# Kernel tuning notes

Hardware: AMD Instinct MI355X
Metric: run time of the kernel (lower is better)

The kernel has to match this reference:

```python
import jax, jax.numpy as jnp
import numpy as np

GROUPS = 32
HEADS = 4
EPS_GN = 1e-5
EPS_DEN = 1e-6


def group_norm(x, gamma, beta):
    b, c, h, w = x.shape
    xg = x.reshape(b, GROUPS, (c // GROUPS) * h * w)
    mu = xg.mean(axis=-1, keepdims=True)
    var = xg.var(axis=-1, keepdims=True)
    xn = ((xg - mu) * jax.lax.rsqrt(var + EPS_GN)).reshape(b, c, h, w)
    return xn * gamma[None, :, None, None] + beta[None, :, None, None]


def setup_inputs() -> dict:
    key = jax.random.key(0)
    ks = jax.random.split(key, 4)
    b, c, h, w = 16, 256, 64, 64
    x = jax.random.normal(ks[0], (b, c, h, w), dtype=jnp.float32)
    gamma = jnp.ones((c,), jnp.float32)
    beta = jnp.zeros((c,), jnp.float32)
    w_qkv = jax.random.normal(ks[1], (3 * c, c), jnp.float32) * (1.0 / np.sqrt(c))
    b_qkv = jnp.zeros((3 * c,), jnp.float32)
    w_out = jax.random.normal(ks[2], (c, c), jnp.float32) * (1.0 / np.sqrt(c))
    b_out = jnp.zeros((c,), jnp.float32)
    return {"x": x, "gamma": gamma, "beta": beta, "w_qkv": w_qkv,
            "b_qkv": b_qkv, "w_out": w_out, "b_out": b_out}


def reference(x, gamma, beta, w_qkv, b_qkv, w_out, b_out):
    b, c, h, w = x.shape
    d = c // HEADS
    n = h * w
    xn = group_norm(x, gamma, beta)
    # 1x1 conv == channel GEMM: [b,3c,h,w]
    qkv = jnp.einsum('bchw,oc->bohw', xn, w_qkv) + b_qkv[None, :, None, None]
    q, k, v = jnp.split(qkv, 3, axis=1)
    # b (heads d) h w -> b heads d n
    q = q.reshape(b, HEADS, d, n)
    k = k.reshape(b, HEADS, d, n)
    v = v.reshape(b, HEADS, d, n)
    q = jax.nn.elu(q) + 1.0
    k = jax.nn.elu(k) + 1.0
    k_sum = k.sum(axis=-1)                                 # [b,H,d]
    kv = jnp.einsum('bhdn,bhen->bhde', k, v)               # [b,H,d,d]
    out = jnp.einsum('bhde,bhdn->bhen', kv, q)             # [b,H,d,n]
    denom = jnp.einsum('bhdn,bhd->bhn', q, k_sum)          # [b,H,n]
    out = out / (denom[:, :, None, :] + EPS_DEN)
    out = out.reshape(b, c, h, w)
    out = jnp.einsum('bchw,oc->bohw', out, w_out) + b_out[None, :, None, None]
    return out + x
```

## Files before the change

### kernel.cpp

```cpp
#include <hip/hip_runtime.h>
#include <stdint.h>

#define BATCH 16
#define CH    256
#define NSP   4096
#define NH    4
#define HD    64

typedef __attribute__((ext_vector_type(8))) short bf16x8;
typedef __attribute__((ext_vector_type(4))) float f32x4;
typedef __attribute__((ext_vector_type(4))) unsigned int u32x4;

__device__ __forceinline__ short f2bf(float f) {
    union { float f; unsigned u; } v; v.f = f;
    unsigned r = (v.u + 0x7fffu + ((v.u >> 16) & 1u)) >> 16;
    return (short)r;
}
__device__ __forceinline__ float bf2f(short s) {
    union { float f; unsigned u; } v; v.u = ((unsigned)(unsigned short)s) << 16;
    return v.f;
}

__global__ __launch_bounds__(256) void k_convert_w(
        const float* __restrict__ wq, const float* __restrict__ wo,
        short* __restrict__ wq_bf, short* __restrict__ wo_bf) {
    int i = blockIdx.x * 256 + threadIdx.x;
    if (i < 768 * 256) wq_bf[i] = f2bf(wq[i]);
    if (i < 256 * 256) wo_bf[i] = f2bf(wo[i]);
}

__global__ __launch_bounds__(256) void k_gn_stats(
        const float* __restrict__ x, float* __restrict__ mu, float* __restrict__ rstd) {
    int bg = blockIdx.x;
    const float4* p = (const float4*)(x + (size_t)bg * 32768);
    float s = 0.f, sq = 0.f;
    for (int i = threadIdx.x; i < 8192; i += 256) {
        float4 v = p[i];
        s  += v.x + v.y + v.z + v.w;
        sq += v.x * v.x + v.y * v.y + v.z * v.z + v.w * v.w;
    }
    for (int off = 32; off; off >>= 1) { s += __shfl_down(s, off); sq += __shfl_down(sq, off); }
    __shared__ float ls[4], lq[4];
    int w = threadIdx.x >> 6;
    if ((threadIdx.x & 63) == 0) { ls[w] = s; lq[w] = sq; }
    __syncthreads();
    if (threadIdx.x == 0) {
        float S = ls[0] + ls[1] + ls[2] + ls[3];
        float Q = lq[0] + lq[1] + lq[2] + lq[3];
        float m = S / 32768.f;
        float var = Q / 32768.f - m * m;
        mu[bg] = m; rstd[bg] = rsqrtf(var + 1e-5f);
    }
}

__global__ __launch_bounds__(256) void k_gn_apply(
        const float* __restrict__ x, const float* __restrict__ gamma,
        const float* __restrict__ beta, const float* __restrict__ mu,
        const float* __restrict__ rstd, short* __restrict__ xn_t) {
    int b = blockIdx.y;
    int n0 = blockIdx.x * 64;
    __shared__ short lds[64 * 264];
    __shared__ float smu[32], srstd[32], sg[256], sb[256];
    int t = threadIdx.x;
    if (t < 32) { smu[t] = mu[b * 32 + t]; srstd[t] = rstd[b * 32 + t]; }
    sg[t] = gamma[t]; sb[t] = beta[t];
    __syncthreads();
    int nl4 = (t & 15) * 4, cq = t >> 4;
    const float* xb = x + (size_t)b * CH * NSP;
    for (int cb = 0; cb < 16; cb++) {
        int c = cb * 16 + cq;
        int g = c >> 3;
        float4 v = *(const float4*)(xb + (size_t)c * NSP + n0 + nl4);
        float sc = srstd[g] * sg[c];
        float sh = sb[c] - smu[g] * sc;
        lds[(nl4 + 0) * 264 + c] = f2bf(v.x * sc + sh);
        lds[(nl4 + 1) * 264 + c] = f2bf(v.y * sc + sh);
        lds[(nl4 + 2) * 264 + c] = f2bf(v.z * sc + sh);
        lds[(nl4 + 3) * 264 + c] = f2bf(v.w * sc + sh);
    }
    __syncthreads();
    short* outb = xn_t + ((size_t)b * NSP + n0) * CH;
    #pragma unroll
    for (int i = 0; i < 8; i++) {
        int ch = t + i * 256;
        int row = ch >> 5, cc = (ch & 31) * 8;
        *(u32x4*)(outb + (size_t)row * CH + cc) = *(const u32x4*)(lds + row * 264 + cc);
    }
}

__global__ __launch_bounds__(256) void k_qkv_gemm(
        const short* __restrict__ wq_bf, const float* __restrict__ b_qkv,
        const short* __restrict__ xn_t, short* __restrict__ q_t,
        float* __restrict__ kvT_g, float* __restrict__ ksum_g) {
    int b = blockIdx.z, mt = blockIdx.y, nt = blockIdx.x;
    bool is_q = (mt < 2);
    int h = mt - 2;
    __shared__ union SM {
        struct { short a[128 * 40]; short bm[128 * 40]; } st;
        short c[128 * 136];
    } sm;
    __shared__ float ksred[64];
    int t = threadIdx.x, lane = t & 63, wv = t >> 6;
    int lr = lane & 15, quad = lane >> 4;
    int wm = (wv & 1) * 64, wn = (wv >> 1) * 64;
    f32x4 acc[4][4] = {};
    const short* Bb = xn_t + ((size_t)b * NSP + (size_t)nt * 128) * 256;
    for (int k0 = 0; k0 < 256; k0 += 32) {
        #pragma unroll
        for (int i = 0; i < 2; i++) {
            int ch = t + i * 256;
            int row = ch >> 2, kc = (ch & 3) * 8;
            int grow = is_q ? (mt * 128 + row)
                            : (row < 64 ? 256 + h * 64 + row : 512 + h * 64 + (row - 64));
            *(u32x4*)(sm.st.a  + row * 40 + kc) = *(const u32x4*)(wq_bf + (size_t)grow * 256 + k0 + kc);
            *(u32x4*)(sm.st.bm + row * 40 + kc) = *(const u32x4*)(Bb + (size_t)row * 256 + k0 + kc);
        }
        __syncthreads();
        bf16x8 afr[4], bfr[4];
        #pragma unroll
        for (int mi = 0; mi < 4; mi++) afr[mi] = *(const bf16x8*)(sm.st.a  + (wm + mi * 16 + lr) * 40 + quad * 8);
        #pragma unroll
        for (int ni = 0; ni < 4; ni++) bfr[ni] = *(const bf16x8*)(sm.st.bm + (wn + ni * 16 + lr) * 40 + quad * 8);
        #pragma unroll
        for (int mi = 0; mi < 4; mi++)
            #pragma unroll
            for (int ni = 0; ni < 4; ni++)
                acc[mi][ni] = __builtin_amdgcn_mfma_f32_16x16x32_bf16(afr[mi], bfr[ni], acc[mi][ni], 0, 0, 0);
        __syncthreads();
    }
    if (t < 64) ksred[t] = 0.f;
    #pragma unroll
    for (int mi = 0; mi < 4; mi++)
      #pragma unroll
      for (int ni = 0; ni < 4; ni++)
        #pragma unroll
        for (int r = 0; r < 4; r++) {
            int ol = wm + mi * 16 + quad * 4 + r;
            int nl = wn + ni * 16 + lr;
            int o = is_q ? (mt * 128 + ol)
                         : (ol < 64 ? 256 + h * 64 + ol : 512 + h * 64 + (ol - 64));
            float v = acc[mi][ni][r] + b_qkv[o];
            if (o < 512) v = v > 0.f ? v + 1.f : __expf(v);
            if (is_q) sm.c[nl * 136 + ol] = f2bf(v);
            else      sm.c[ol * 136 + nl] = f2bf(v);
        }
    __syncthreads();
    if (is_q) {
        short* qb = q_t + (size_t)b * NH * NSP * HD;
        #pragma unroll
        for (int i = 0; i < 8; i++) {
            int ch = t + i * 256;
            int row = ch >> 4, c8 = (ch & 15) * 8;
            int hh = mt * 2 + (c8 >> 6), d0 = c8 & 63;
            int n = nt * 128 + row;
            *(u32x4*)(qb + ((size_t)hh * NSP + n) * HD + d0) = *(const u32x4*)(sm.c + row * 136 + c8);
        }
    } else {
        {
            int kd = t >> 2, nc0 = (t & 3) * 32;
            float s = 0.f;
            #pragma unroll
            for (int j = 0; j < 32; j++) s += bf2f(sm.c[kd * 136 + nc0 + j]);
            atomicAdd(&ksred[kd], s);
        }
        f32x4 acc2[4] = {};
        #pragma unroll
        for (int kk = 0; kk < 128; kk += 32) {
            bf16x8 af = *(const bf16x8*)(sm.c + (64 + wv * 16 + lr) * 136 + kk + quad * 8);
            bf16x8 bf[4];
            #pragma unroll
            for (int ni = 0; ni < 4; ni++)
                bf[ni] = *(const bf16x8*)(sm.c + (ni * 16 + lr) * 136 + kk + quad * 8);
            #pragma unroll
            for (int ni = 0; ni < 4; ni++)
                acc2[ni] = __builtin_amdgcn_mfma_f32_16x16x32_bf16(af, bf[ni], acc2[ni], 0, 0, 0);
        }
        __syncthreads();
        int bh = b * NH + h;
        float* kvg = kvT_g + (size_t)bh * 4096;
        #pragma unroll
        for (int ni = 0; ni < 4; ni++)
            #pragma unroll
            for (int r = 0; r < 4; r++) {
                int e = wv * 16 + quad * 4 + r;
                int d = ni * 16 + lr;
                atomicAdd(&kvg[e * 64 + d], acc2[ni][r]);
            }
        if (t < 64) atomicAdd(&ksum_g[bh * 64 + t], ksred[t]);
    }
}

__global__ __launch_bounds__(256) void k_attn(
        const short* __restrict__ q_t, const float* __restrict__ kvT_g,
        const float* __restrict__ ksum_g, short* __restrict__ attn_t) {
    int nt = blockIdx.x, h = blockIdx.y, b = blockIdx.z;
    int bh = b * 4 + h;
    __shared__ short ql[128 * 72];
    __shared__ short kvl[64 * 72];
    __shared__ float ksl[64];
    __shared__ float dnl[128];
    int t = threadIdx.x, lane = t & 63, wv = t >> 6, lr = lane & 15, quad = lane >> 4;
    const short* qb = q_t + ((size_t)bh * NSP + (size_t)nt * 128) * HD;
    #pragma unroll
    for (int i = 0; i < 4; i++) {
        int ch = t + i * 256;
        int row = ch >> 3, dc = (ch & 7) * 8;
        *(u32x4*)(ql + row * 72 + dc) = *(const u32x4*)(qb + (size_t)row * HD + dc);
    }
    const float* kvg = kvT_g + (size_t)bh * 4096;
    for (int i = t; i < 4096; i += 256)
        kvl[(i >> 6) * 72 + (i & 63)] = f2bf(kvg[i]);
    if (t < 64) ksl[t] = ksum_g[bh * 64 + t];
    __syncthreads();
    if (t < 128) {
        float s = 0.f;
        #pragma unroll
        for (int d = 0; d < 64; d++) s += bf2f(ql[t * 72 + d]) * ksl[d];
        dnl[t] = 1.f / (s + 1e-6f);
    }
    __syncthreads();
    f32x4 acc[2][4] = {};
    int mbase = wv * 32;
    #pragma unroll
    for (int kk = 0; kk < 64; kk += 32) {
        bf16x8 afr[2], bfr[4];
        #pragma unroll
        for (int mi = 0; mi < 2; mi++) afr[mi] = *(const bf16x8*)(ql + (mbase + mi * 16 + lr) * 72 + kk + quad * 8);
        #pragma unroll
        for (int ni = 0; ni < 4; ni++) bfr[ni] = *(const bf16x8*)(kvl + (ni * 16 + lr) * 72 + kk + quad * 8);
        #pragma unroll
        for (int mi = 0; mi < 2; mi++)
            #pragma unroll
            for (int ni = 0; ni < 4; ni++)
                acc[mi][ni] = __builtin_amdgcn_mfma_f32_16x16x32_bf16(afr[mi], bfr[ni], acc[mi][ni], 0, 0, 0);
    }
    short* ob = attn_t + ((size_t)b * NSP + (size_t)nt * 128) * CH + h * 64;
    #pragma unroll
    for (int mi = 0; mi < 2; mi++)
      #pragma unroll
      for (int ni = 0; ni < 4; ni++)
        #pragma unroll
        for (int r = 0; r < 4; r++) {
            int nl = mbase + mi * 16 + quad * 4 + r;
            int e = ni * 16 + lr;
            ob[(size_t)nl * CH + e] = f2bf(acc[mi][ni][r] * dnl[nl]);
        }
}

__global__ __launch_bounds__(256) void k_out_gemm(
        const short* __restrict__ wo_bf, const float* __restrict__ b_out,
        const short* __restrict__ attn_t, const float* __restrict__ x,
        float* __restrict__ out) {
    int b = blockIdx.z, mt = blockIdx.y, nt = blockIdx.x;
    __shared__ short lds_a[128 * 40];
    __shared__ short lds_b[128 * 40];
    int t = threadIdx.x, lane = t & 63, wv = t >> 6, lr = lane & 15, quad = lane >> 4;
    int wm = (wv & 1) * 64, wn = (wv >> 1) * 64;
    f32x4 acc[4][4] = {};
    const short* Ab = wo_bf + (size_t)mt * 128 * 256;
    const short* Bb = attn_t + ((size_t)b * NSP + (size_t)nt * 128) * 256;
    for (int k0 = 0; k0 < 256; k0 += 32) {
        #pragma unroll
        for (int i = 0; i < 2; i++) {
            int ch = t + i * 256;
            int row = ch >> 2, kc = (ch & 3) * 8;
            *(u32x4*)(lds_a + row * 40 + kc) = *(const u32x4*)(Ab + (size_t)row * 256 + k0 + kc);
            *(u32x4*)(lds_b + row * 40 + kc) = *(const u32x4*)(Bb + (size_t)row * 256 + k0 + kc);
        }
        __syncthreads();
        bf16x8 afr[4], bfr[4];
        #pragma unroll
        for (int mi = 0; mi < 4; mi++) afr[mi] = *(const bf16x8*)(lds_a + (wm + mi * 16 + lr) * 40 + quad * 8);
        #pragma unroll
        for (int ni = 0; ni < 4; ni++) bfr[ni] = *(const bf16x8*)(lds_b + (wn + ni * 16 + lr) * 40 + quad * 8);
        #pragma unroll
        for (int mi = 0; mi < 4; mi++)
            #pragma unroll
            for (int ni = 0; ni < 4; ni++)
                acc[mi][ni] = __builtin_amdgcn_mfma_f32_16x16x32_bf16(afr[mi], bfr[ni], acc[mi][ni], 0, 0, 0);
        __syncthreads();
    }
    const float* xb = x + ((size_t)b * CH + (size_t)mt * 128) * NSP + (size_t)nt * 128;
    float* outb = out + ((size_t)b * CH + (size_t)mt * 128) * NSP + (size_t)nt * 128;
    #pragma unroll
    for (int mi = 0; mi < 4; mi++)
      #pragma unroll
      for (int ni = 0; ni < 4; ni++)
        #pragma unroll
        for (int r = 0; r < 4; r++) {
            int ol = wm + mi * 16 + quad * 4 + r;
            int nl = wn + ni * 16 + lr;
            int o = mt * 128 + ol;
            outb[(size_t)ol * NSP + nl] = acc[mi][ni][r] + b_out[o] + xb[(size_t)ol * NSP + nl];
        }
}

extern "C" void kernel_launch(void* const* d_in, const int* in_sizes, int n_in,
                              void* d_out, int out_size, void* d_ws, size_t ws_size,
                              hipStream_t stream) {
    const float* x     = (const float*)d_in[0];
    const float* gamma = (const float*)d_in[1];
    const float* beta  = (const float*)d_in[2];
    const float* w_qkv = (const float*)d_in[3];
    const float* b_qkv = (const float*)d_in[4];
    const float* w_out = (const float*)d_in[5];
    const float* b_out = (const float*)d_in[6];
    float* out = (float*)d_out;

    char* ws = (char*)d_ws;
    size_t off = 0;
    float* mu    = (float*)(ws + off); off += 2048;
    float* rstd  = (float*)(ws + off); off += 2048;
    short* wq_bf = (short*)(ws + off); off += (size_t)768 * 256 * 2;
    short* wo_bf = (short*)(ws + off); off += (size_t)256 * 256 * 2;
    short* xn_t  = (short*)(ws + off);
    short* attn_t = xn_t;
    off += (size_t)BATCH * NSP * CH * 2;
    short* q_t   = (short*)(ws + off); off += (size_t)BATCH * NSP * CH * 2;
    float* kvT_g = (float*)(ws + off); off += (size_t)64 * 4096 * 4;
    float* ksum_g = (float*)(ws + off); off += (size_t)64 * 64 * 4;

    if (ws_size < off) return;

    k_convert_w<<<768, 256, 0, stream>>>(w_qkv, w_out, wq_bf, wo_bf);
    k_gn_stats<<<512, 256, 0, stream>>>(x, mu, rstd);
    k_gn_apply<<<dim3(64, 16), 256, 0, stream>>>(x, gamma, beta, mu, rstd, xn_t);
    hipMemsetAsync(kvT_g, 0, (size_t)(64 * 4096 + 64 * 64) * 4, stream);
    k_qkv_gemm<<<dim3(32, 6, 16), 256, 0, stream>>>(wq_bf, b_qkv, xn_t, q_t, kvT_g, ksum_g);
    k_attn<<<dim3(32, 4, 16), 256, 0, stream>>>(q_t, kvT_g, ksum_g, attn_t);
    k_out_gemm<<<dim3(32, 2, 16), 256, 0, stream>>>(wo_bf, b_out, attn_t, x, out);
}
```

Before: 311.1 us.

## Fuse GroupNorm into QKV GEMM and attention into output GEMM

Merges weight conversion with GN stats into one pre-kernel, and applies GroupNorm directly into LDS inside the QKV GEMM so the bf16 xn intermediate is never written out. KV partials are now written per tile and reduced by a separate kernel instead of global atomics and a memset. Attention is computed per 64-column tile for all heads into LDS and fed straight into the output projection, removing the attn_t round trip. In exchange there are fewer blocks (1024 per fused kernel), serialized per-head loops with many barriers, and a large kvp partial buffer (64 MB) that must be written and then read back.

```diff
diff --git a/kernel.cpp b/kernel.cpp
--- a/kernel.cpp
+++ b/kernel.cpp
@@ -21,278 +21,317 @@
     return v.f;
 }
 
-__global__ __launch_bounds__(256) void k_convert_w(
-        const float* __restrict__ wq, const float* __restrict__ wo,
+__global__ __launch_bounds__(256) void k_pre(
+        const float* __restrict__ x, const float* __restrict__ wq, const float* __restrict__ wo,
+        float* __restrict__ mu, float* __restrict__ rstd,
         short* __restrict__ wq_bf, short* __restrict__ wo_bf) {
-    int i = blockIdx.x * 256 + threadIdx.x;
-    if (i < 768 * 256) wq_bf[i] = f2bf(wq[i]);
-    if (i < 256 * 256) wo_bf[i] = f2bf(wo[i]);
-}
-
-__global__ __launch_bounds__(256) void k_gn_stats(
-        const float* __restrict__ x, float* __restrict__ mu, float* __restrict__ rstd) {
     int bg = blockIdx.x;
-    const float4* p = (const float4*)(x + (size_t)bg * 32768);
-    float s = 0.f, sq = 0.f;
-    for (int i = threadIdx.x; i < 8192; i += 256) {
-        float4 v = p[i];
-        s  += v.x + v.y + v.z + v.w;
-        sq += v.x * v.x + v.y * v.y + v.z * v.z + v.w * v.w;
-    }
-    for (int off = 32; off; off >>= 1) { s += __shfl_down(s, off); sq += __shfl_down(sq, off); }
-    __shared__ float ls[4], lq[4];
-    int w = threadIdx.x >> 6;
-    if ((threadIdx.x & 63) == 0) { ls[w] = s; lq[w] = sq; }
+    if (bg < 512) {
+        const float4* p = (const float4*)(x + (size_t)bg * 32768);
+        float s = 0.f, sq = 0.f;
+        for (int i = threadIdx.x; i < 8192; i += 256) {
+            float4 v = p[i];
+            s  += v.x + v.y + v.z + v.w;
+            sq += v.x * v.x + v.y * v.y + v.z * v.z + v.w * v.w;
+        }
+        for (int off = 32; off; off >>= 1) { s += __shfl_down(s, off); sq += __shfl_down(sq, off); }
+        __shared__ float ls[4], lq[4];
+        int w = threadIdx.x >> 6;
+        if ((threadIdx.x & 63) == 0) { ls[w] = s; lq[w] = sq; }
+        __syncthreads();
+        if (threadIdx.x == 0) {
+            float S = ls[0] + ls[1] + ls[2] + ls[3];
+            float Q = lq[0] + lq[1] + lq[2] + lq[3];
+            float m = S / 32768.f;
+            float var = Q / 32768.f - m * m;
+            mu[bg] = m; rstd[bg] = rsqrtf(var + 1e-5f);
+        }
+    } else {
+        int idx = ((bg - 512) * 256 + threadIdx.x) * 4;
+        float4 v;
+        short* dst;
+        if (idx < 196608) { v = *(const float4*)(wq + idx); dst = wq_bf + idx; }
+        else              { v = *(const float4*)(wo + (idx - 196608)); dst = wo_bf + (idx - 196608); }
+        unsigned p0 = ((unsigned)(unsigned short)f2bf(v.x)) | (((unsigned)(unsigned short)f2bf(v.y)) << 16);
+        unsigned p1 = ((unsigned)(unsigned short)f2bf(v.z)) | (((unsigned)(unsigned short)f2bf(v.w)) << 16);
+        uint2 pk; pk.x = p0; pk.y = p1;
+        *(uint2*)dst = pk;
+    }
+}
+
+__global__ __launch_bounds__(256) void k_gnqkv(
+        const float* __restrict__ x, const float* __restrict__ gamma, const float* __restrict__ beta,
+        const float* __restrict__ mu, const float* __restrict__ rstd,
+        const short* __restrict__ wq_bf, const float* __restrict__ b_qkv,
+        short* __restrict__ q_t, float* __restrict__ kvp, float* __restrict__ ksp) {
+    int b = blockIdx.y, nt = blockIdx.x;
+    int n0 = nt * 64;
+    __shared__ short Blds[64 * 264];
+    __shared__ short Asm[128 * 40];
+    __shared__ union UR {
+        struct { short kst[64 * 72]; short vst[64 * 72]; } s;
+        short cst[64 * 136];
+    } R;
+    int t = threadIdx.x, lane = t & 63, wv = t >> 6, lr = lane & 15, quad = lane >> 4;
+
+    {
+        const float* xb = x + (size_t)b * CH * NSP;
+        int m = t & 15, cq = t >> 4;
+        for (int cb = 0; cb < 16; cb++) {
+            int c = cb * 16 + cq;
+            int g = c >> 3;
+            float sc = rstd[b * 32 + g] * gamma[c];
+            float sh = beta[c] - mu[b * 32 + g] * sc;
+            float4 v = *(const float4*)(xb + (size_t)c * NSP + n0 + m * 4);
+            float vv[4] = {v.x, v.y, v.z, v.w};
+            #pragma unroll
+            for (int j = 0; j < 4; j++) {
+                int n = m * 4 + j;
+                int cc = c ^ (((n >> 4) & 3) << 3);
+                Blds[n * 264 + cc] = f2bf(vv[j] * sc + sh);
+            }
+        }
+    }
     __syncthreads();
-    if (threadIdx.x == 0) {
-        float S = ls[0] + ls[1] + ls[2] + ls[3];
-        float Q = lq[0] + lq[1] + lq[2] + lq[3];
-        float m = S / 32768.f;
-        float var = Q / 32768.f - m * m;
-        mu[bg] = m; rstd[bg] = rsqrtf(var + 1e-5f);
-    }
-}
-
-__global__ __launch_bounds__(256) void k_gn_apply(
-        const float* __restrict__ x, const float* __restrict__ gamma,
-        const float* __restrict__ beta, const float* __restrict__ mu,
-        const float* __restrict__ rstd, short* __restrict__ xn_t) {
-    int b = blockIdx.y;
-    int n0 = blockIdx.x * 64;
-    __shared__ short lds[64 * 264];
-    __shared__ float smu[32], srstd[32], sg[256], sb[256];
+
+    for (int h = 0; h < 4; h++) {
+        for (int pass = 0; pass < 2; pass++) {
+            int base = (pass ? 512 : 256) + h * 64;
+            f32x4 acc[2][2] = {};
+            int wm = (wv & 1) * 32, wn = (wv >> 1) * 32;
+            for (int k0 = 0; k0 < 256; k0 += 32) {
+                int row = t >> 2, kc = (t & 3) * 8;
+                *(u32x4*)(Asm + row * 40 + kc) = *(const u32x4*)(wq_bf + (size_t)(base + row) * 256 + k0 + kc);
+                __syncthreads();
+                bf16x8 afr[2], bfr[2];
+                #pragma unroll
+                for (int mi = 0; mi < 2; mi++) afr[mi] = *(const bf16x8*)(Asm + (wm + mi * 16 + lr) * 40 + quad * 8);
+                #pragma unroll
+                for (int ni = 0; ni < 2; ni++) {
+                    int rr = wn + ni * 16 + lr;
+                    bfr[ni] = *(const bf16x8*)(Blds + rr * 264 + ((k0 + quad * 8) ^ (((rr >> 4) & 3) << 3)));
+                }
+                #pragma unroll
+                for (int mi = 0; mi < 2; mi++)
+                    #pragma unroll
+                    for (int ni = 0; ni < 2; ni++)
+                        acc[mi][ni] = __builtin_amdgcn_mfma_f32_16x16x32_bf16(afr[mi], bfr[ni], acc[mi][ni], 0, 0, 0);
+                __syncthreads();
+            }
+            short* dst = pass ? R.s.vst : R.s.kst;
+            #pragma unroll
+            for (int mi = 0; mi < 2; mi++)
+              #pragma unroll
+              for (int ni = 0; ni < 2; ni++)
+                #pragma unroll
+                for (int r = 0; r < 4; r++) {
+                    int ol = wm + mi * 16 + quad * 4 + r;
+                    int nl = wn + ni * 16 + lr;
+                    float v = acc[mi][ni][r] + b_qkv[base + ol];
+                    if (!pass) v = v > 0.f ? v + 1.f : __expf(v);
+                    dst[ol * 72 + nl] = f2bf(v);
+                }
+            __syncthreads();
+            if (!pass) {
+                int d = t >> 2, nq = (t & 3) * 16;
+                float s = 0.f;
+                #pragma unroll
+                for (int j = 0; j < 16; j++) s += bf2f(R.s.kst[d * 72 + nq + j]);
+                s += __shfl_down(s, 2);
+                s += __shfl_down(s, 1);
+                if ((t & 3) == 0) ksp[((size_t)(b * 4 + h) * 64 + nt) * 64 + d] = s;
+            }
+        }
+        f32x4 acc2[4] = {};
+        #pragma unroll
+        for (int kk = 0; kk < 64; kk += 32) {
+            bf16x8 af = *(const bf16x8*)(R.s.vst + (wv * 16 + lr) * 72 + kk + quad * 8);
+            bf16x8 bfk[4];
+            #pragma unroll
+            for (int ni = 0; ni < 4; ni++)
+                bfk[ni] = *(const bf16x8*)(R.s.kst + (ni * 16 + lr) * 72 + kk + quad * 8);
+            #pragma unroll
+            for (int ni = 0; ni < 4; ni++)
+                acc2[ni] = __builtin_amdgcn_mfma_f32_16x16x32_bf16(af, bfk[ni], acc2[ni], 0, 0, 0);
+        }
+        float* kvdst = kvp + ((size_t)(b * 4 + h) * 64 + nt) * 4096;
+        #pragma unroll
+        for (int ni = 0; ni < 4; ni++)
+            #pragma unroll
+            for (int r = 0; r < 4; r++)
+                kvdst[(wv * 16 + quad * 4 + r) * 64 + ni * 16 + lr] = acc2[ni][r];
+    }
+
+    for (int mtq = 0; mtq < 2; mtq++) {
+        f32x4 acc[4][2] = {};
+        int wm = (wv & 1) * 64, wn = (wv >> 1) * 32;
+        for (int k0 = 0; k0 < 256; k0 += 32) {
+            #pragma unroll
+            for (int i = 0; i < 2; i++) {
+                int ch = t + i * 256;
+                int row = ch >> 2, kc = (ch & 3) * 8;
+                *(u32x4*)(Asm + row * 40 + kc) = *(const u32x4*)(wq_bf + (size_t)(mtq * 128 + row) * 256 + k0 + kc);
+            }
+            __syncthreads();
+            bf16x8 afr[4], bfr[2];
+            #pragma unroll
+            for (int mi = 0; mi < 4; mi++) afr[mi] = *(const bf16x8*)(Asm + (wm + mi * 16 + lr) * 40 + quad * 8);
+            #pragma unroll
+            for (int ni = 0; ni < 2; ni++) {
+                int rr = wn + ni * 16 + lr;
+                bfr[ni] = *(const bf16x8*)(Blds + rr * 264 + ((k0 + quad * 8) ^ (((rr >> 4) & 3) << 3)));
+            }
+            #pragma unroll
+            for (int mi = 0; mi < 4; mi++)
+                #pragma unroll
+                for (int ni = 0; ni < 2; ni++)
+                    acc[mi][ni] = __builtin_amdgcn_mfma_f32_16x16x32_bf16(afr[mi], bfr[ni], acc[mi][ni], 0, 0, 0);
+            __syncthreads();
+        }
+        #pragma unroll
+        for (int mi = 0; mi < 4; mi++)
+          #pragma unroll
+          for (int ni = 0; ni < 2; ni++)
+            #pragma unroll
+            for (int r = 0; r < 4; r++) {
+                int ol = wm + mi * 16 + quad * 4 + r;
+                int nl = wn + ni * 16 + lr;
+                float v = acc[mi][ni][r] + b_qkv[mtq * 128 + ol];
+                v = v > 0.f ? v + 1.f : __expf(v);
+                R.cst[nl * 136 + ol] = f2bf(v);
+            }
+        __syncthreads();
+        #pragma unroll
+        for (int i = 0; i < 4; i++) {
+            int ch = t + i * 256;
+            int row = ch >> 4, o8 = (ch & 15) * 8;
+            int hh = mtq * 2 + (o8 >> 6), d0 = o8 & 63;
+            *(u32x4*)(q_t + ((size_t)(b * 4 + hh) * NSP + n0 + row) * HD + d0) =
+                *(const u32x4*)(R.cst + row * 136 + o8);
+        }
+        __syncthreads();
+    }
+}
+
+__global__ __launch_bounds__(256) void k_kv_reduce(
+        const float* __restrict__ kvp, const float* __restrict__ ksp,
+        float* __restrict__ kvT_g, float* __restrict__ ksum_g) {
+    int eq = blockIdx.x, bh = blockIdx.y;
     int t = threadIdx.x;
-    if (t < 32) { smu[t] = mu[b * 32 + t]; srstd[t] = rstd[b * 32 + t]; }
-    sg[t] = gamma[t]; sb[t] = beta[t];
-    __syncthreads();
-    int nl4 = (t & 15) * 4, cq = t >> 4;
-    const float* xb = x + (size_t)b * CH * NSP;
-    for (int cb = 0; cb < 16; cb++) {
-        int c = cb * 16 + cq;
-        int g = c >> 3;
-        float4 v = *(const float4*)(xb + (size_t)c * NSP + n0 + nl4);
-        float sc = srstd[g] * sg[c];
-        float sh = sb[c] - smu[g] * sc;
-        lds[(nl4 + 0) * 264 + c] = f2bf(v.x * sc + sh);
-        lds[(nl4 + 1) * 264 + c] = f2bf(v.y * sc + sh);
-        lds[(nl4 + 2) * 264 + c] = f2bf(v.z * sc + sh);
-        lds[(nl4 + 3) * 264 + c] = f2bf(v.w * sc + sh);
-    }
-    __syncthreads();
-    short* outb = xn_t + ((size_t)b * NSP + n0) * CH;
-    #pragma unroll
-    for (int i = 0; i < 8; i++) {
-        int ch = t + i * 256;
-        int row = ch >> 5, cc = (ch & 31) * 8;
-        *(u32x4*)(outb + (size_t)row * CH + cc) = *(const u32x4*)(lds + row * 264 + cc);
-    }
-}
-
-__global__ __launch_bounds__(256) void k_qkv_gemm(
-        const short* __restrict__ wq_bf, const float* __restrict__ b_qkv,
-        const short* __restrict__ xn_t, short* __restrict__ q_t,
-        float* __restrict__ kvT_g, float* __restrict__ ksum_g) {
-    int b = blockIdx.z, mt = blockIdx.y, nt = blockIdx.x;
-    bool is_q = (mt < 2);
-    int h = mt - 2;
-    __shared__ union SM {
-        struct { short a[128 * 40]; short bm[128 * 40]; } st;
-        short c[128 * 136];
-    } sm;
-    __shared__ float ksred[64];
-    int t = threadIdx.x, lane = t & 63, wv = t >> 6;
-    int lr = lane & 15, quad = lane >> 4;
-    int wm = (wv & 1) * 64, wn = (wv >> 1) * 64;
-    f32x4 acc[4][4] = {};
-    const short* Bb = xn_t + ((size_t)b * NSP + (size_t)nt * 128) * 256;
-    for (int k0 = 0; k0 < 256; k0 += 32) {
+    const float* base = kvp + (size_t)bh * 64 * 4096 + eq * 1024;
+    float4 s = {0.f, 0.f, 0.f, 0.f};
+    for (int ntc = 0; ntc < 64; ntc++) {
+        float4 v = *(const float4*)(base + (size_t)ntc * 4096 + t * 4);
+        s.x += v.x; s.y += v.y; s.z += v.z; s.w += v.w;
+    }
+    *(float4*)(kvT_g + (size_t)bh * 4096 + eq * 1024 + t * 4) = s;
+    if (eq == 0 && t < 64) {
+        float ss = 0.f;
+        for (int ntc = 0; ntc < 64; ntc++) ss += ksp[((size_t)bh * 64 + ntc) * 64 + t];
+        ksum_g[bh * 64 + t] = ss;
+    }
+}
+
+__global__ __launch_bounds__(256) void k_attn_out(
+        const short* __restrict__ q_t, const float* __restrict__ kvT_g,
+        const float* __restrict__ ksum_g, const short* __restrict__ wo_bf,
+        const float* __restrict__ b_out, const float* __restrict__ x,
+        float* __restrict__ out) {
+    int b = blockIdx.y, nt = blockIdx.x;
+    int n0 = nt * 64;
+    __shared__ short Battn[64 * 264];
+    __shared__ union UR {
+        struct { short ql[64 * 72]; short kvl[64 * 72]; } a;
+        short Asm2[128 * 40];
+    } R;
+    __shared__ float ksl[64], dnl[64];
+    int t = threadIdx.x, lane = t & 63, wv = t >> 6, lr = lane & 15, quad = lane >> 4;
+
+    for (int h = 0; h < 4; h++) {
+        int bh = b * 4 + h;
         #pragma unroll
         for (int i = 0; i < 2; i++) {
             int ch = t + i * 256;
-            int row = ch >> 2, kc = (ch & 3) * 8;
-            int grow = is_q ? (mt * 128 + row)
-                            : (row < 64 ? 256 + h * 64 + row : 512 + h * 64 + (row - 64));
-            *(u32x4*)(sm.st.a  + row * 40 + kc) = *(const u32x4*)(wq_bf + (size_t)grow * 256 + k0 + kc);
-            *(u32x4*)(sm.st.bm + row * 40 + kc) = *(const u32x4*)(Bb + (size_t)row * 256 + k0 + kc);
-        }
-        __syncthreads();
-        bf16x8 afr[4], bfr[4];
-        #pragma unroll
-        for (int mi = 0; mi < 4; mi++) afr[mi] = *(const bf16x8*)(sm.st.a  + (wm + mi * 16 + lr) * 40 + quad * 8);
-        #pragma unroll
-        for (int ni = 0; ni < 4; ni++) bfr[ni] = *(const bf16x8*)(sm.st.bm + (wn + ni * 16 + lr) * 40 + quad * 8);
+            int row = ch >> 3, dc = (ch & 7) * 8;
+            *(u32x4*)(R.a.ql + row * 72 + dc) =
+                *(const u32x4*)(q_t + ((size_t)bh * NSP + n0 + row) * HD + dc);
+        }
+        const float* kvg = kvT_g + (size_t)bh * 4096;
+        for (int i = t; i < 4096; i += 256)
+            R.a.kvl[(i >> 6) * 72 + (i & 63)] = f2bf(kvg[i]);
+        if (t < 64) ksl[t] = ksum_g[bh * 64 + t];
+        __syncthreads();
+        if (t < 64) {
+            float s = 0.f;
+            #pragma unroll
+            for (int d = 0; d < 64; d++) s += bf2f(R.a.ql[t * 72 + d]) * ksl[d];
+            dnl[t] = 1.f / (s + 1e-6f);
+        }
+        __syncthreads();
+        f32x4 acc[4] = {};
+        #pragma unroll
+        for (int kk = 0; kk < 64; kk += 32) {
+            bf16x8 af = *(const bf16x8*)(R.a.ql + (wv * 16 + lr) * 72 + kk + quad * 8);
+            bf16x8 bfr[4];
+            #pragma unroll
+            for (int ni = 0; ni < 4; ni++)
+                bfr[ni] = *(const bf16x8*)(R.a.kvl + (ni * 16 + lr) * 72 + kk + quad * 8);
+            #pragma unroll
+            for (int ni = 0; ni < 4; ni++)
+                acc[ni] = __builtin_amdgcn_mfma_f32_16x16x32_bf16(af, bfr[ni], acc[ni], 0, 0, 0);
+        }
+        float dn[4];
+        #pragma unroll
+        for (int r = 0; r < 4; r++) dn[r] = dnl[wv * 16 + quad * 4 + r];
+        #pragma unroll
+        for (int ni = 0; ni < 4; ni++)
+            #pragma unroll
+            for (int r = 0; r < 4; r++) {
+                int n = wv * 16 + quad * 4 + r;
+                int e = ni * 16 + lr;
+                Battn[n * 264 + h * 64 + e] = f2bf(acc[ni][r] * dn[r]);
+            }
+        __syncthreads();
+    }
+
+    for (int p = 0; p < 2; p++) {
+        f32x4 acc[4][2] = {};
+        int wm = (wv & 1) * 64, wn = (wv >> 1) * 32;
+        for (int k0 = 0; k0 < 256; k0 += 32) {
+            #pragma unroll
+            for (int i = 0; i < 2; i++) {
+                int ch = t + i * 256;
+                int row = ch >> 2, kc = (ch & 3) * 8;
+                *(u32x4*)(R.Asm2 + row * 40 + kc) =
+                    *(const u32x4*)(wo_bf + (size_t)(p * 128 + row) * 256 + k0 + kc);
+            }
+            __syncthreads();
+            bf16x8 afr[4], bfr[2];
+            #pragma unroll
+            for (int mi = 0; mi < 4; mi++) afr[mi] = *(const bf16x8*)(R.Asm2 + (wm + mi * 16 + lr) * 40 + quad * 8);
+            #pragma unroll
+            for (int ni = 0; ni < 2; ni++)
+                bfr[ni] = *(const bf16x8*)(Battn + (wn + ni * 16 + lr) * 264 + k0 + quad * 8);
+            #pragma unroll
+            for (int mi = 0; mi < 4; mi++)
+                #pragma unroll
+                for (int ni = 0; ni < 2; ni++)
+                    acc[mi][ni] = __builtin_amdgcn_mfma_f32_16x16x32_bf16(afr[mi], bfr[ni], acc[mi][ni], 0, 0, 0);
+            __syncthreads();
+        }
         #pragma unroll
         for (int mi = 0; mi < 4; mi++)
-            #pragma unroll
-            for (int ni = 0; ni < 4; ni++)
-                acc[mi][ni] = __builtin_amdgcn_mfma_f32_16x16x32_bf16(afr[mi], bfr[ni], acc[mi][ni], 0, 0, 0);
-        __syncthreads();
-    }
-    if (t < 64) ksred[t] = 0.f;
-    #pragma unroll
-    for (int mi = 0; mi < 4; mi++)
-      #pragma unroll
-      for (int ni = 0; ni < 4; ni++)
-        #pragma unroll
-        for (int r = 0; r < 4; r++) {
-            int ol = wm + mi * 16 + quad * 4 + r;
-            int nl = wn + ni * 16 + lr;
-            int o = is_q ? (mt * 128 + ol)
-                         : (ol < 64 ? 256 + h * 64 + ol : 512 + h * 64 + (ol - 64));
-            float v = acc[mi][ni][r] + b_qkv[o];
-            if (o < 512) v = v > 0.f ? v + 1.f : __expf(v);
-            if (is_q) sm.c[nl * 136 + ol] = f2bf(v);
-            else      sm.c[ol * 136 + nl] = f2bf(v);
-        }
-    __syncthreads();
-    if (is_q) {
-        short* qb = q_t + (size_t)b * NH * NSP * HD;
-        #pragma unroll
-        for (int i = 0; i < 8; i++) {
-            int ch = t + i * 256;
-            int row = ch >> 4, c8 = (ch & 15) * 8;
-            int hh = mt * 2 + (c8 >> 6), d0 = c8 & 63;
-            int n = nt * 128 + row;
-            *(u32x4*)(qb + ((size_t)hh * NSP + n) * HD + d0) = *(const u32x4*)(sm.c + row * 136 + c8);
-        }
-    } else {
-        {
-            int kd = t >> 2, nc0 = (t & 3) * 32;
-            float s = 0.f;
-            #pragma unroll
-            for (int j = 0; j < 32; j++) s += bf2f(sm.c[kd * 136 + nc0 + j]);
-            atomicAdd(&ksred[kd], s);
-        }
-        f32x4 acc2[4] = {};
-        #pragma unroll
-        for (int kk = 0; kk < 128; kk += 32) {
-            bf16x8 af = *(const bf16x8*)(sm.c + (64 + wv * 16 + lr) * 136 + kk + quad * 8);
-            bf16x8 bf[4];
-            #pragma unroll
-            for (int ni = 0; ni < 4; ni++)
-                bf[ni] = *(const bf16x8*)(sm.c + (ni * 16 + lr) * 136 + kk + quad * 8);
-            #pragma unroll
-            for (int ni = 0; ni < 4; ni++)
-                acc2[ni] = __builtin_amdgcn_mfma_f32_16x16x32_bf16(af, bf[ni], acc2[ni], 0, 0, 0);
-        }
-        __syncthreads();
-        int bh = b * NH + h;
-        float* kvg = kvT_g + (size_t)bh * 4096;
-        #pragma unroll
-        for (int ni = 0; ni < 4; ni++)
+          #pragma unroll
+          for (int ni = 0; ni < 2; ni++)
             #pragma unroll
             for (int r = 0; r < 4; r++) {
-                int e = wv * 16 + quad * 4 + r;
-                int d = ni * 16 + lr;
-                atomicAdd(&kvg[e * 64 + d], acc2[ni][r]);
-            }
-        if (t < 64) atomicAdd(&ksum_g[bh * 64 + t], ksred[t]);
-    }
-}
-
-__global__ __launch_bounds__(256) void k_attn(
-        const short* __restrict__ q_t, const float* __restrict__ kvT_g,
-        const float* __restrict__ ksum_g, short* __restrict__ attn_t) {
-    int nt = blockIdx.x, h = blockIdx.y, b = blockIdx.z;
-    int bh = b * 4 + h;
-    __shared__ short ql[128 * 72];
-    __shared__ short kvl[64 * 72];
-    __shared__ float ksl[64];
-    __shared__ float dnl[128];
-    int t = threadIdx.x, lane = t & 63, wv = t >> 6, lr = lane & 15, quad = lane >> 4;
-    const short* qb = q_t + ((size_t)bh * NSP + (size_t)nt * 128) * HD;
-    #pragma unroll
-    for (int i = 0; i < 4; i++) {
-        int ch = t + i * 256;
-        int row = ch >> 3, dc = (ch & 7) * 8;
-        *(u32x4*)(ql + row * 72 + dc) = *(const u32x4*)(qb + (size_t)row * HD + dc);
-    }
-    const float* kvg = kvT_g + (size_t)bh * 4096;
-    for (int i = t; i < 4096; i += 256)
-        kvl[(i >> 6) * 72 + (i & 63)] = f2bf(kvg[i]);
-    if (t < 64) ksl[t] = ksum_g[bh * 64 + t];
-    __syncthreads();
-    if (t < 128) {
-        float s = 0.f;
-        #pragma unroll
-        for (int d = 0; d < 64; d++) s += bf2f(ql[t * 72 + d]) * ksl[d];
-        dnl[t] = 1.f / (s + 1e-6f);
-    }
-    __syncthreads();
-    f32x4 acc[2][4] = {};
-    int mbase = wv * 32;
-    #pragma unroll
-    for (int kk = 0; kk < 64; kk += 32) {
-        bf16x8 afr[2], bfr[4];
-        #pragma unroll
-        for (int mi = 0; mi < 2; mi++) afr[mi] = *(const bf16x8*)(ql + (mbase + mi * 16 + lr) * 72 + kk + quad * 8);
-        #pragma unroll
-        for (int ni = 0; ni < 4; ni++) bfr[ni] = *(const bf16x8*)(kvl + (ni * 16 + lr) * 72 + kk + quad * 8);
-        #pragma unroll
-        for (int mi = 0; mi < 2; mi++)
-            #pragma unroll
-            for (int ni = 0; ni < 4; ni++)
-                acc[mi][ni] = __builtin_amdgcn_mfma_f32_16x16x32_bf16(afr[mi], bfr[ni], acc[mi][ni], 0, 0, 0);
-    }
-    short* ob = attn_t + ((size_t)b * NSP + (size_t)nt * 128) * CH + h * 64;
-    #pragma unroll
-    for (int mi = 0; mi < 2; mi++)
-      #pragma unroll
-      for (int ni = 0; ni < 4; ni++)
-        #pragma unroll
-        for (int r = 0; r < 4; r++) {
-            int nl = mbase + mi * 16 + quad * 4 + r;
-            int e = ni * 16 + lr;
-            ob[(size_t)nl * CH + e] = f2bf(acc[mi][ni][r] * dnl[nl]);
-        }
-}
-
-__global__ __launch_bounds__(256) void k_out_gemm(
-        const short* __restrict__ wo_bf, const float* __restrict__ b_out,
-        const short* __restrict__ attn_t, const float* __restrict__ x,
-        float* __restrict__ out) {
-    int b = blockIdx.z, mt = blockIdx.y, nt = blockIdx.x;
-    __shared__ short lds_a[128 * 40];
-    __shared__ short lds_b[128 * 40];
-    int t = threadIdx.x, lane = t & 63, wv = t >> 6, lr = lane & 15, quad = lane >> 4;
-    int wm = (wv & 1) * 64, wn = (wv >> 1) * 64;
-    f32x4 acc[4][4] = {};
-    const short* Ab = wo_bf + (size_t)mt * 128 * 256;
-    const short* Bb = attn_t + ((size_t)b * NSP + (size_t)nt * 128) * 256;
-    for (int k0 = 0; k0 < 256; k0 += 32) {
-        #pragma unroll
-        for (int i = 0; i < 2; i++) {
-            int ch = t + i * 256;
-            int row = ch >> 2, kc = (ch & 3) * 8;
-            *(u32x4*)(lds_a + row * 40 + kc) = *(const u32x4*)(Ab + (size_t)row * 256 + k0 + kc);
-            *(u32x4*)(lds_b + row * 40 + kc) = *(const u32x4*)(Bb + (size_t)row * 256 + k0 + kc);
-        }
-        __syncthreads();
-        bf16x8 afr[4], bfr[4];
-        #pragma unroll
-        for (int mi = 0; mi < 4; mi++) afr[mi] = *(const bf16x8*)(lds_a + (wm + mi * 16 + lr) * 40 + quad * 8);
-        #pragma unroll
-        for (int ni = 0; ni < 4; ni++) bfr[ni] = *(const bf16x8*)(lds_b + (wn + ni * 16 + lr) * 40 + quad * 8);
-        #pragma unroll
-        for (int mi = 0; mi < 4; mi++)
-            #pragma unroll
-            for (int ni = 0; ni < 4; ni++)
-                acc[mi][ni] = __builtin_amdgcn_mfma_f32_16x16x32_bf16(afr[mi], bfr[ni], acc[mi][ni], 0, 0, 0);
-        __syncthreads();
-    }
-    const float* xb = x + ((size_t)b * CH + (size_t)mt * 128) * NSP + (size_t)nt * 128;
-    float* outb = out + ((size_t)b * CH + (size_t)mt * 128) * NSP + (size_t)nt * 128;
-    #pragma unroll
-    for (int mi = 0; mi < 4; mi++)
-      #pragma unroll
-      for (int ni = 0; ni < 4; ni++)
-        #pragma unroll
-        for (int r = 0; r < 4; r++) {
-            int ol = wm + mi * 16 + quad * 4 + r;
-            int nl = wn + ni * 16 + lr;
-            int o = mt * 128 + ol;
-            outb[(size_t)ol * NSP + nl] = acc[mi][ni][r] + b_out[o] + xb[(size_t)ol * NSP + nl];
-        }
+                int ol = wm + mi * 16 + quad * 4 + r;
+                int nl = wn + ni * 16 + lr;
+                int o = p * 128 + ol;
+                size_t idx = ((size_t)b * CH + o) * NSP + n0 + nl;
+                out[idx] = acc[mi][ni][r] + b_out[o] + x[idx];
+            }
+    }
 }
 
 extern "C" void kernel_launch(void* const* d_in, const int* in_sizes, int n_in,
@@ -313,20 +352,16 @@
     float* rstd  = (float*)(ws + off); off += 2048;
     short* wq_bf = (short*)(ws + off); off += (size_t)768 * 256 * 2;
     short* wo_bf = (short*)(ws + off); off += (size_t)256 * 256 * 2;
-    short* xn_t  = (short*)(ws + off);
-    short* attn_t = xn_t;
-    off += (size_t)BATCH * NSP * CH * 2;
     short* q_t   = (short*)(ws + off); off += (size_t)BATCH * NSP * CH * 2;
+    float* kvp   = (float*)(ws + off); off += (size_t)64 * 64 * 4096 * 4;
+    float* ksp   = (float*)(ws + off); off += (size_t)64 * 64 * 64 * 4;
     float* kvT_g = (float*)(ws + off); off += (size_t)64 * 4096 * 4;
     float* ksum_g = (float*)(ws + off); off += (size_t)64 * 64 * 4;
 
     if (ws_size < off) return;
 
-    k_convert_w<<<768, 256, 0, stream>>>(w_qkv, w_out, wq_bf, wo_bf);
-    k_gn_stats<<<512, 256, 0, stream>>>(x, mu, rstd);
-    k_gn_apply<<<dim3(64, 16), 256, 0, stream>>>(x, gamma, beta, mu, rstd, xn_t);
-    hipMemsetAsync(kvT_g, 0, (size_t)(64 * 4096 + 64 * 64) * 4, stream);
-    k_qkv_gemm<<<dim3(32, 6, 16), 256, 0, stream>>>(wq_bf, b_qkv, xn_t, q_t, kvT_g, ksum_g);
-    k_attn<<<dim3(32, 4, 16), 256, 0, stream>>>(q_t, kvT_g, ksum_g, attn_t);
-    k_out_gemm<<<dim3(32, 2, 16), 256, 0, stream>>>(wo_bf, b_out, attn_t, x, out);
-}
+    k_pre<<<768, 256, 0, stream>>>(x, w_qkv, w_out, mu, rstd, wq_bf, wo_bf);
+    k_gnqkv<<<dim3(64, 16), 256, 0, stream>>>(x, gamma, beta, mu, rstd, wq_bf, b_qkv, q_t, kvp, ksp);
+    k_kv_reduce<<<dim3(4, 64), 256, 0, stream>>>(kvp, ksp, kvT_g, ksum_g);
+    k_attn_out<<<dim3(64, 16), 256, 0, stream>>>(q_t, kvT_g, ksum_g, wo_bf, b_out, x, out);
+}
```

New measurement: 283.2 us. 9.0% less time.
